# Performance work log

Measured on AMD Instinct MI355X. Metric: run time of the kernel, lower is better.

Reference implementation:

```python
import jax, jax.numpy as jnp
import numpy as np

TOP_K = 2  # active_experts


def setup_inputs() -> dict:
    key = jax.random.key(0)
    k0, k1, k2, k3 = jax.random.split(key, 4)
    B, S, D, E, H = 4, 1024, 2048, 16, 1024
    x = jax.random.normal(k0, (B, S, D), jnp.float32) * 0.02
    Wg = jax.random.normal(k1, (E, D), jnp.float32) * 0.02          # gate: Linear(dim, E, bias=False)
    balance_bias = jnp.zeros((E,), jnp.float32)                      # registered buffer, init zeros
    W1 = jax.random.normal(k2, (E, D, H), jnp.float32) * 0.02        # expert up-proj (no bias)
    W2 = jax.random.normal(k3, (E, H, D), jnp.float32) * 0.02        # expert down-proj (no bias)
    return {"x": x, "Wg": Wg, "balance_bias": balance_bias, "W1": W1, "W2": W2}


def reference(x, Wg, balance_bias, W1, W2):
    B, S, D = x.shape
    E = Wg.shape[0]
    xf = x.reshape(-1, D)                                   # [T, D], T = B*S
    T = xf.shape[0]

    # sigmoid gating with load-balance bias
    gate_logits = xf @ Wg.T                                 # [T, E]
    gate_scores = jax.nn.sigmoid(gate_logits + balance_bias)

    # top-k selection + normalization (matches torch.topk + sum-normalize)
    topk_scores, topk_idx = jax.lax.top_k(gate_scores, TOP_K)
    topk_scores = topk_scores / (topk_scores.sum(-1, keepdims=True) + 1e-6)

    # dense combine weights [T, E]: zero for unselected experts -> identical math
    # to the per-expert masked index_add in the original module
    combine = jnp.zeros((T, E), xf.dtype).at[jnp.arange(T)[:, None], topk_idx].add(topk_scores)

    # per-expert FFN: SiLU(x W1_e) W2_e, weighted-combined across experts
    h = jax.nn.silu(jnp.einsum('td,edh->teh', xf, W1))      # [T, E, H]
    out = jnp.einsum('teh,te,ehd->td', h, combine, W2)      # [T, D]
    return out.reshape(B, S, D)
```

## Files before the change

### kernel.cpp

```cpp
#include <hip/hip_runtime.h>
#include <math.h>

#define T_TOK 4096
#define DDIM  2048
#define HDIM  1024
#define NEXP  16
#define CAP   4096
#define GBM   128
#define GBN   128
#define GBK   64
#define MAX_TILES 80

typedef __attribute__((ext_vector_type(8))) short  short8;
typedef __attribute__((ext_vector_type(4))) float  floatx4;

__device__ __forceinline__ unsigned short f2bf(float f) {
    unsigned int u = __float_as_uint(f);
    u += 0x7fffu + ((u >> 16) & 1u);
    return (unsigned short)(u >> 16);
}
__device__ __forceinline__ float bf2f(unsigned short u) {
    return __uint_as_float((unsigned int)u << 16);
}

__device__ __forceinline__ void gl_lds16(const void* g, void* l) {
    __builtin_amdgcn_global_load_lds(
        (const __attribute__((address_space(1))) unsigned int*)g,
        (__attribute__((address_space(3))) unsigned int*)l,
        16, 0, 0);
}

__global__ __launch_bounds__(256) void prep_kernel(
    const float* __restrict__ x, const float* __restrict__ Wg,
    const float* __restrict__ bias,
    const float* __restrict__ W1, const float* __restrict__ W2,
    unsigned short* __restrict__ W1T, unsigned short* __restrict__ W2T,
    int* __restrict__ counts, int* __restrict__ tok_list,
    int4* __restrict__ tinfo, float2* __restrict__ wcomb,
    unsigned short* __restrict__ xbf)
{
    __shared__ __align__(16) unsigned short Tt[64][72];
    int z = blockIdx.z;

    if (z < 32) {
        const float* src; unsigned short* dst; int K, N, kt, nt;
        if (z < NEXP) {
            K = DDIM; N = HDIM;
            src = W1 + (size_t)z * K * N;
            dst = W1T + (size_t)z * (size_t)N * K;
            kt = blockIdx.y * 64; nt = blockIdx.x * 64;
        } else {
            K = HDIM; N = DDIM;
            src = W2 + (size_t)(z - NEXP) * K * N;
            dst = W2T + (size_t)(z - NEXP) * (size_t)N * K;
            kt = blockIdx.x * 64; nt = blockIdx.y * 64;
        }
        int tid = threadIdx.x;
        int r = tid >> 4, c4 = (tid & 15) * 4;
        const float* s = src + (size_t)kt * N + nt;
#pragma unroll
        for (int i = 0; i < 4; ++i) {
            int rr = r + i * 16;
            float4 v = *(const float4*)(s + (size_t)rr * N + c4);
            Tt[c4 + 0][rr] = f2bf(v.x); Tt[c4 + 1][rr] = f2bf(v.y);
            Tt[c4 + 2][rr] = f2bf(v.z); Tt[c4 + 3][rr] = f2bf(v.w);
        }
        __syncthreads();
        unsigned short* d = dst + (size_t)nt * K + kt;
#pragma unroll
        for (int it = 0; it < 2; ++it) {
            int c = tid + it * 256;
            int n = c >> 3, kc = c & 7;
            short8 v = *(const short8*)&Tt[n][kc * 8];
            *(short8*)(d + (size_t)n * K + kc * 8) = v;
        }
        return;
    }

    int tb   = (z - 32) * 512 + blockIdx.y * 16 + blockIdx.x;
    int wv   = threadIdx.x >> 6;
    int lane = threadIdx.x & 63;
    int t    = tb * 4 + wv;

    const float4* xp4 = (const float4*)x + (size_t)t * (DDIM / 4);
    ushort4* xbp4 = (ushort4*)(xbf + (size_t)t * DDIM);
    const float4* wg4 = (const float4*)Wg;

    float acc[NEXP];
#pragma unroll
    for (int e = 0; e < NEXP; ++e) acc[e] = 0.f;

    for (int it = 0; it < DDIM / 4 / 64; ++it) {
        int d4 = it * 64 + lane;
        float4 xv = xp4[d4];
        ushort4 xs;
        xs.x = f2bf(xv.x); xs.y = f2bf(xv.y);
        xs.z = f2bf(xv.z); xs.w = f2bf(xv.w);
        xbp4[d4] = xs;
#pragma unroll
        for (int e = 0; e < NEXP; ++e) {
            float4 wvv = wg4[e * (DDIM / 4) + d4];
            acc[e] += xv.x * wvv.x + xv.y * wvv.y + xv.z * wvv.z + xv.w * wvv.w;
        }
    }
#pragma unroll
    for (int e = 0; e < NEXP; ++e) {
        float v = acc[e];
#pragma unroll
        for (int off = 32; off > 0; off >>= 1) v += __shfl_xor(v, off, 64);
        acc[e] = v;
    }
    if (lane == 0) {
        float s[NEXP];
#pragma unroll
        for (int e = 0; e < NEXP; ++e)
            s[e] = 1.f / (1.f + expf(-(acc[e] + bias[e])));
        int i0 = 0;
#pragma unroll
        for (int e = 1; e < NEXP; ++e) if (s[e] > s[i0]) i0 = e;
        int i1 = (i0 == 0) ? 1 : 0;
        for (int e = 0; e < NEXP; ++e)
            if (e != i0 && s[e] > s[i1]) i1 = e;
        float denom = s[i0] + s[i1] + 1e-6f;
        int p0 = atomicAdd(&counts[i0], 1);
        tok_list[i0 * CAP + p0] = t;
        int p1 = atomicAdd(&counts[i1], 1);
        tok_list[i1 * CAP + p1] = t;
        tinfo[t] = make_int4(i0, p0, i1, p1);
        wcomb[t] = make_float2(s[i0] / denom, s[i1] / denom);
    }
}

__global__ void scan_kernel(const int* __restrict__ counts, int* __restrict__ offsets,
                            int* __restrict__ ntiles, int* __restrict__ tile_e,
                            int* __restrict__ tile_mt)
{
    if (threadIdx.x == 0 && blockIdx.x == 0) {
        int s = 0, nt = 0;
        for (int e = 0; e < NEXP; ++e) {
            offsets[e] = s;
            int c = counts[e];
            s += c;
            for (int mt = 0; mt * GBM < c; ++mt) {
                tile_e[nt] = e; tile_mt[nt] = mt; ++nt;
            }
        }
        offsets[NEXP] = s;
        *ntiles = nt;
    }
}

__global__ __launch_bounds__(256) void up_gemm(
    const unsigned short* __restrict__ xbf, const unsigned short* __restrict__ W1T,
    const int* __restrict__ counts, const int* __restrict__ offsets,
    const int* __restrict__ ntiles, const int* __restrict__ tile_e,
    const int* __restrict__ tile_mt,
    const int* __restrict__ tok_list, unsigned short* __restrict__ hbuf)
{
    int idx = blockIdx.x;
    if (idx >= *ntiles) return;
    int e   = tile_e[idx];
    int mt  = tile_mt[idx];
    int cnt = counts[e];
    int nbase = blockIdx.y * GBN;

    __shared__ __align__(16) unsigned short As[2][GBM * GBK];
    __shared__ __align__(16) unsigned short Bs[2][GBN * GBK];

    int tid = threadIdx.x, lane = tid & 63, wv = tid >> 6;
    int kcL = ((lane & 7) ^ ((lane >> 3) & 7)) * 8;
    int hbase = offsets[e];

    const unsigned short* gA[4];
    const unsigned short* gB[4];
#pragma unroll
    for (int j = 0; j < 4; ++j) {
        int row = wv * 32 + j * 8 + (lane >> 3);
        int m = mt * GBM + row; if (m >= cnt) m = cnt - 1;
        int tok = tok_list[e * CAP + m];
        gA[j] = xbf + (size_t)tok * DDIM + kcL;
        gB[j] = W1T + ((size_t)e * HDIM + nbase + row) * DDIM + kcL;
    }
    int fr = lane & 15, fq = lane >> 4;
    int wm = (wv & 1) * 64, wn = (wv >> 1) * 64;

    floatx4 acc[4][4];
#pragma unroll
    for (int i = 0; i < 4; ++i)
#pragma unroll
        for (int j = 0; j < 4; ++j) acc[i][j] = (floatx4){0.f, 0.f, 0.f, 0.f};

#pragma unroll
    for (int j = 0; j < 4; ++j)
        gl_lds16(gA[j], &As[0][((wv * 4 + j) * 64 + lane) * 8]);
#pragma unroll
    for (int j = 0; j < 4; ++j)
        gl_lds16(gB[j], &Bs[0][((wv * 4 + j) * 64 + lane) * 8]);

    const int NK = DDIM / GBK;
    for (int i = 0; i < NK; ++i) {
        int cur = i & 1, nxt = cur ^ 1;
        __syncthreads();
        if (i + 1 < NK) {
            int k0 = (i + 1) * GBK;
#pragma unroll
            for (int j = 0; j < 4; ++j)
                gl_lds16(gA[j] + k0, &As[nxt][((wv * 4 + j) * 64 + lane) * 8]);
#pragma unroll
            for (int j = 0; j < 4; ++j)
                gl_lds16(gB[j] + k0, &Bs[nxt][((wv * 4 + j) * 64 + lane) * 8]);
        }
#pragma unroll
        for (int ks = 0; ks < 2; ++ks) {
            short8 af[4], bfr[4];
#pragma unroll
            for (int mi = 0; mi < 4; ++mi) {
                int row = wm + mi * 16 + fr;
                int kcs = (ks * 4 + fq) ^ (row & 7);
                af[mi] = *(const short8*)&As[cur][row * GBK + kcs * 8];
            }
#pragma unroll
            for (int ni = 0; ni < 4; ++ni) {
                int row = wn + ni * 16 + fr;
                int kcs = (ks * 4 + fq) ^ (row & 7);
                bfr[ni] = *(const short8*)&Bs[cur][row * GBK + kcs * 8];
            }
#pragma unroll
            for (int mi = 0; mi < 4; ++mi)
#pragma unroll
                for (int ni = 0; ni < 4; ++ni)
                    acc[mi][ni] = __builtin_amdgcn_mfma_f32_16x16x32_bf16(
                        af[mi], bfr[ni], acc[mi][ni], 0, 0, 0);
        }
    }

#pragma unroll
    for (int mi = 0; mi < 4; ++mi) {
#pragma unroll
        for (int r = 0; r < 4; ++r) {
            int row = wm + mi * 16 + fq * 4 + r;
            int m = mt * GBM + row;
            if (m < cnt) {
                size_t ro = (size_t)(hbase + m) * HDIM + nbase + wn;
#pragma unroll
                for (int ni = 0; ni < 4; ++ni) {
                    float u  = acc[mi][ni][r];
                    float hh = u / (1.f + __expf(-u));
                    hbuf[ro + ni * 16 + fr] = f2bf(hh);
                }
            }
        }
    }
}

__global__ __launch_bounds__(256) void down_gemm(
    const unsigned short* __restrict__ hbuf, const unsigned short* __restrict__ W2T,
    const int* __restrict__ counts, const int* __restrict__ offsets,
    const int* __restrict__ ntiles, const int* __restrict__ tile_e,
    const int* __restrict__ tile_mt,
    unsigned short* __restrict__ ybuf)
{
    int idx = blockIdx.x;
    if (idx >= *ntiles) return;
    int e   = tile_e[idx];
    int mt  = tile_mt[idx];
    int cnt = counts[e];
    int nbase = blockIdx.y * GBN;

    __shared__ __align__(16) unsigned short As[2][GBM * GBK];
    __shared__ __align__(16) unsigned short Bs[2][GBN * GBK];

    int tid = threadIdx.x, lane = tid & 63, wv = tid >> 6;
    int kcL = ((lane & 7) ^ ((lane >> 3) & 7)) * 8;
    int hbase = offsets[e];

    const unsigned short* gA[4];
    const unsigned short* gB[4];
#pragma unroll
    for (int j = 0; j < 4; ++j) {
        int row = wv * 32 + j * 8 + (lane >> 3);
        int m = mt * GBM + row; if (m >= cnt) m = cnt - 1;
        gA[j] = hbuf + (size_t)(hbase + m) * HDIM + kcL;
        gB[j] = W2T + ((size_t)e * DDIM + nbase + row) * HDIM + kcL;
    }
    int fr = lane & 15, fq = lane >> 4;
    int wm = (wv & 1) * 64, wn = (wv >> 1) * 64;

    floatx4 acc[4][4];
#pragma unroll
    for (int i = 0; i < 4; ++i)
#pragma unroll
        for (int j = 0; j < 4; ++j) acc[i][j] = (floatx4){0.f, 0.f, 0.f, 0.f};

#pragma unroll
    for (int j = 0; j < 4; ++j)
        gl_lds16(gA[j], &As[0][((wv * 4 + j) * 64 + lane) * 8]);
#pragma unroll
    for (int j = 0; j < 4; ++j)
        gl_lds16(gB[j], &Bs[0][((wv * 4 + j) * 64 + lane) * 8]);

    const int NK = HDIM / GBK;
    for (int i = 0; i < NK; ++i) {
        int cur = i & 1, nxt = cur ^ 1;
        __syncthreads();
        if (i + 1 < NK) {
            int k0 = (i + 1) * GBK;
#pragma unroll
            for (int j = 0; j < 4; ++j)
                gl_lds16(gA[j] + k0, &As[nxt][((wv * 4 + j) * 64 + lane) * 8]);
#pragma unroll
            for (int j = 0; j < 4; ++j)
                gl_lds16(gB[j] + k0, &Bs[nxt][((wv * 4 + j) * 64 + lane) * 8]);
        }
#pragma unroll
        for (int ks = 0; ks < 2; ++ks) {
            short8 af[4], bfr[4];
#pragma unroll
            for (int mi = 0; mi < 4; ++mi) {
                int row = wm + mi * 16 + fr;
                int kcs = (ks * 4 + fq) ^ (row & 7);
                af[mi] = *(const short8*)&As[cur][row * GBK + kcs * 8];
            }
#pragma unroll
            for (int ni = 0; ni < 4; ++ni) {
                int row = wn + ni * 16 + fr;
                int kcs = (ks * 4 + fq) ^ (row & 7);
                bfr[ni] = *(const short8*)&Bs[cur][row * GBK + kcs * 8];
            }
#pragma unroll
            for (int mi = 0; mi < 4; ++mi)
#pragma unroll
                for (int ni = 0; ni < 4; ++ni)
                    acc[mi][ni] = __builtin_amdgcn_mfma_f32_16x16x32_bf16(
                        af[mi], bfr[ni], acc[mi][ni], 0, 0, 0);
        }
    }

#pragma unroll
    for (int mi = 0; mi < 4; ++mi) {
#pragma unroll
        for (int r = 0; r < 4; ++r) {
            int row = wm + mi * 16 + fq * 4 + r;
            int m = mt * GBM + row;
            if (m < cnt) {
                size_t ro = (size_t)(hbase + m) * DDIM + nbase + wn;
#pragma unroll
                for (int ni = 0; ni < 4; ++ni)
                    ybuf[ro + ni * 16 + fr] = f2bf(acc[mi][ni][r]);
            }
        }
    }
}

__global__ __launch_bounds__(256) void combine_kernel(
    const unsigned short* __restrict__ ybuf, const int* __restrict__ offsets,
    const int4* __restrict__ tinfo, const float2* __restrict__ wcomb,
    float* __restrict__ out)
{
    int t = blockIdx.x;
    int4   ti = tinfo[t];
    float2 w  = wcomb[t];
    int s0 = offsets[ti.x] + ti.y;
    int s1 = offsets[ti.z] + ti.w;
    const ushort4* y0 = (const ushort4*)(ybuf + (size_t)s0 * DDIM);
    const ushort4* y1 = (const ushort4*)(ybuf + (size_t)s1 * DDIM);
    float4* op = (float4*)(out + (size_t)t * DDIM);
#pragma unroll
    for (int i = 0; i < 2; ++i) {
        int c = threadIdx.x + i * 256;
        ushort4 a = y0[c], b = y1[c];
        float4 r;
        r.x = w.x * bf2f(a.x) + w.y * bf2f(b.x);
        r.y = w.x * bf2f(a.y) + w.y * bf2f(b.y);
        r.z = w.x * bf2f(a.z) + w.y * bf2f(b.z);
        r.w = w.x * bf2f(a.w) + w.y * bf2f(b.w);
        op[c] = r;
    }
}

extern "C" void kernel_launch(void* const* d_in, const int* in_sizes, int n_in,
                              void* d_out, int out_size, void* d_ws, size_t ws_size,
                              hipStream_t stream)
{
    const float* x    = (const float*)d_in[0];
    const float* Wg   = (const float*)d_in[1];
    const float* bias = (const float*)d_in[2];
    const float* W1   = (const float*)d_in[3];
    const float* W2   = (const float*)d_in[4];
    float* out = (float*)d_out;

    char* ws = (char*)d_ws;
    int*            counts   = (int*)(ws + 0);
    int*            offsets  = (int*)(ws + 256);
    int*            ntiles   = (int*)(ws + 512);
    int*            tile_e   = (int*)(ws + 512 + 4);
    int*            tile_mt  = (int*)(ws + 512 + 4 + MAX_TILES * 4);
    int*            tok_list = (int*)(ws + 2048);
    int4*           tinfo    = (int4*)(ws + 264192);
    float2*         wcomb    = (float2*)(ws + 329728);
    unsigned short* xbf      = (unsigned short*)(ws + 524288);
    unsigned short* hbuf     = (unsigned short*)(ws + 17301504);
    unsigned short* ybuf     = (unsigned short*)(ws + 34078720);
    unsigned short* W1T      = (unsigned short*)(ws + 67633152);
    unsigned short* W2T      = (unsigned short*)(ws + 134742016);

    hipMemsetAsync(counts, 0, 64, stream);

    prep_kernel<<<dim3(16, 32, 34), 256, 0, stream>>>(
        x, Wg, bias, W1, W2, W1T, W2T, counts, tok_list, tinfo, wcomb, xbf);
    scan_kernel<<<1, 64, 0, stream>>>(counts, offsets, ntiles, tile_e, tile_mt);
    up_gemm<<<dim3(MAX_TILES, HDIM / GBN), 256, 0, stream>>>(
        xbf, W1T, counts, offsets, ntiles, tile_e, tile_mt, tok_list, hbuf);
    down_gemm<<<dim3(MAX_TILES, DDIM / GBN), 256, 0, stream>>>(
        hbuf, W2T, counts, offsets, ntiles, tile_e, tile_mt, ybuf);
    combine_kernel<<<T_TOK, 256, 0, stream>>>(ybuf, offsets, tinfo, wcomb, out);
}
```

Before: 652.2 us.

## Enlarge weight-transpose tiles with swizzled LDS and parallelize routing scan

The weight transpose/bf16 conversion in prep_kernel now processes 256x64 tiles per block instead of 64x64. It packs four k-values per uint2 into an XOR-swizzled LDS layout and writes wider contiguous runs of 512 bytes per row. The gating part now handles 16 tokens per block instead of 4, and the grid shrinks from 17408 blocks to 4352. The single-thread scan kernel is replaced with a wavefront shuffle prefix sum. The aim is to cut the many small blocks, the LDS bank conflicts and the narrow global writes in the weight conversion, at the cost of more LDS per block and possible occupancy or load-balance changes.

```diff
diff --git a/kernel.cpp b/kernel.cpp
--- a/kernel.cpp
+++ b/kernel.cpp
@@ -39,95 +39,114 @@
     int4* __restrict__ tinfo, float2* __restrict__ wcomb,
     unsigned short* __restrict__ xbf)
 {
-    __shared__ __align__(16) unsigned short Tt[64][72];
-    int z = blockIdx.z;
-
-    if (z < 32) {
+    __shared__ __align__(16) unsigned short Ls[64 * 256];
+    int z   = blockIdx.z;
+    int bid = blockIdx.x;
+    int tid = threadIdx.x;
+
+    if (bid < 128) {
         const float* src; unsigned short* dst; int K, N, kt, nt;
         if (z < NEXP) {
             K = DDIM; N = HDIM;
             src = W1 + (size_t)z * K * N;
             dst = W1T + (size_t)z * (size_t)N * K;
-            kt = blockIdx.y * 64; nt = blockIdx.x * 64;
+            kt = bid >> 4; nt = bid & 15;
         } else {
             K = HDIM; N = DDIM;
             src = W2 + (size_t)(z - NEXP) * K * N;
             dst = W2T + (size_t)(z - NEXP) * (size_t)N * K;
-            kt = blockIdx.x * 64; nt = blockIdx.y * 64;
-        }
-        int tid = threadIdx.x;
-        int r = tid >> 4, c4 = (tid & 15) * 4;
-        const float* s = src + (size_t)kt * N + nt;
-#pragma unroll
-        for (int i = 0; i < 4; ++i) {
-            int rr = r + i * 16;
-            float4 v = *(const float4*)(s + (size_t)rr * N + c4);
-            Tt[c4 + 0][rr] = f2bf(v.x); Tt[c4 + 1][rr] = f2bf(v.y);
-            Tt[c4 + 2][rr] = f2bf(v.z); Tt[c4 + 3][rr] = f2bf(v.w);
+            kt = bid >> 5; nt = bid & 31;
+        }
+        int kb = kt * 256, nb = nt * 64;
+        int r = tid >> 4;
+        int c16 = tid & 15;
+        const float* s0 = src + (size_t)kb * N + nb + c16 * 4;
+
+#pragma unroll
+        for (int i4 = 0; i4 < 4; ++i4) {
+            float4 v[4];
+#pragma unroll
+            for (int i = 0; i < 4; ++i)
+                v[i] = *(const float4*)(s0 + (size_t)(i4 * 64 + r * 4 + i) * N);
+#pragma unroll
+            for (int j = 0; j < 4; ++j) {
+                unsigned int lo = (unsigned int)f2bf(((const float*)&v[0])[j])
+                                | ((unsigned int)f2bf(((const float*)&v[1])[j]) << 16);
+                unsigned int hi = (unsigned int)f2bf(((const float*)&v[2])[j])
+                                | ((unsigned int)f2bf(((const float*)&v[3])[j]) << 16);
+                int n  = c16 * 4 + j;
+                int g  = i4 * 16 + r;
+                int gp = g ^ (n & 14);
+                *(uint2*)&Ls[n * 256 + gp * 4] = make_uint2(lo, hi);
+            }
         }
         __syncthreads();
-        unsigned short* d = dst + (size_t)nt * K + kt;
-#pragma unroll
-        for (int it = 0; it < 2; ++it) {
-            int c = tid + it * 256;
-            int n = c >> 3, kc = c & 7;
-            short8 v = *(const short8*)&Tt[n][kc * 8];
-            *(short8*)(d + (size_t)n * K + kc * 8) = v;
+        unsigned short* d0 = dst + (size_t)nb * K + kb;
+#pragma unroll
+        for (int j = 0; j < 8; ++j) {
+            int c = tid + j * 256;
+            int n = c >> 5, a = c & 31;
+            int sp = (2 * a) ^ (n & 14);
+            short8 sv = *(const short8*)&Ls[n * 256 + sp * 4];
+            *(short8*)(d0 + (size_t)n * K + a * 8) = sv;
         }
         return;
     }
 
-    int tb   = (z - 32) * 512 + blockIdx.y * 16 + blockIdx.x;
-    int wv   = threadIdx.x >> 6;
-    int lane = threadIdx.x & 63;
-    int t    = tb * 4 + wv;
-
-    const float4* xp4 = (const float4*)x + (size_t)t * (DDIM / 4);
-    ushort4* xbp4 = (ushort4*)(xbf + (size_t)t * DDIM);
+    int gb   = z * 8 + (bid - 128);
+    int wv   = tid >> 6;
+    int lane = tid & 63;
     const float4* wg4 = (const float4*)Wg;
 
-    float acc[NEXP];
-#pragma unroll
-    for (int e = 0; e < NEXP; ++e) acc[e] = 0.f;
-
-    for (int it = 0; it < DDIM / 4 / 64; ++it) {
-        int d4 = it * 64 + lane;
-        float4 xv = xp4[d4];
-        ushort4 xs;
-        xs.x = f2bf(xv.x); xs.y = f2bf(xv.y);
-        xs.z = f2bf(xv.z); xs.w = f2bf(xv.w);
-        xbp4[d4] = xs;
+    for (int tk = 0; tk < 4; ++tk) {
+        int t = gb * 16 + wv * 4 + tk;
+
+        const float4* xp4 = (const float4*)x + (size_t)t * (DDIM / 4);
+        ushort4* xbp4 = (ushort4*)(xbf + (size_t)t * DDIM);
+
+        float acc[NEXP];
+#pragma unroll
+        for (int e = 0; e < NEXP; ++e) acc[e] = 0.f;
+
+        for (int it = 0; it < DDIM / 4 / 64; ++it) {
+            int d4 = it * 64 + lane;
+            float4 xv = xp4[d4];
+            ushort4 xs;
+            xs.x = f2bf(xv.x); xs.y = f2bf(xv.y);
+            xs.z = f2bf(xv.z); xs.w = f2bf(xv.w);
+            xbp4[d4] = xs;
+#pragma unroll
+            for (int e = 0; e < NEXP; ++e) {
+                float4 wvv = wg4[e * (DDIM / 4) + d4];
+                acc[e] += xv.x * wvv.x + xv.y * wvv.y + xv.z * wvv.z + xv.w * wvv.w;
+            }
+        }
 #pragma unroll
         for (int e = 0; e < NEXP; ++e) {
-            float4 wvv = wg4[e * (DDIM / 4) + d4];
-            acc[e] += xv.x * wvv.x + xv.y * wvv.y + xv.z * wvv.z + xv.w * wvv.w;
-        }
-    }
-#pragma unroll
-    for (int e = 0; e < NEXP; ++e) {
-        float v = acc[e];
-#pragma unroll
-        for (int off = 32; off > 0; off >>= 1) v += __shfl_xor(v, off, 64);
-        acc[e] = v;
-    }
-    if (lane == 0) {
-        float s[NEXP];
-#pragma unroll
-        for (int e = 0; e < NEXP; ++e)
-            s[e] = 1.f / (1.f + expf(-(acc[e] + bias[e])));
-        int i0 = 0;
-#pragma unroll
-        for (int e = 1; e < NEXP; ++e) if (s[e] > s[i0]) i0 = e;
-        int i1 = (i0 == 0) ? 1 : 0;
-        for (int e = 0; e < NEXP; ++e)
-            if (e != i0 && s[e] > s[i1]) i1 = e;
-        float denom = s[i0] + s[i1] + 1e-6f;
-        int p0 = atomicAdd(&counts[i0], 1);
-        tok_list[i0 * CAP + p0] = t;
-        int p1 = atomicAdd(&counts[i1], 1);
-        tok_list[i1 * CAP + p1] = t;
-        tinfo[t] = make_int4(i0, p0, i1, p1);
-        wcomb[t] = make_float2(s[i0] / denom, s[i1] / denom);
+            float v = acc[e];
+#pragma unroll
+            for (int off = 32; off > 0; off >>= 1) v += __shfl_xor(v, off, 64);
+            acc[e] = v;
+        }
+        if (lane == 0) {
+            float s[NEXP];
+#pragma unroll
+            for (int e = 0; e < NEXP; ++e)
+                s[e] = 1.f / (1.f + expf(-(acc[e] + bias[e])));
+            int i0 = 0;
+#pragma unroll
+            for (int e = 1; e < NEXP; ++e) if (s[e] > s[i0]) i0 = e;
+            int i1 = (i0 == 0) ? 1 : 0;
+            for (int e = 0; e < NEXP; ++e)
+                if (e != i0 && s[e] > s[i1]) i1 = e;
+            float denom = s[i0] + s[i1] + 1e-6f;
+            int p0 = atomicAdd(&counts[i0], 1);
+            tok_list[i0 * CAP + p0] = t;
+            int p1 = atomicAdd(&counts[i1], 1);
+            tok_list[i1 * CAP + p1] = t;
+            tinfo[t] = make_int4(i0, p0, i1, p1);
+            wcomb[t] = make_float2(s[i0] / denom, s[i1] / denom);
+        }
     }
 }
 
@@ -135,18 +154,31 @@
                             int* __restrict__ ntiles, int* __restrict__ tile_e,
                             int* __restrict__ tile_mt)
 {
-    if (threadIdx.x == 0 && blockIdx.x == 0) {
-        int s = 0, nt = 0;
-        for (int e = 0; e < NEXP; ++e) {
-            offsets[e] = s;
-            int c = counts[e];
-            s += c;
-            for (int mt = 0; mt * GBM < c; ++mt) {
-                tile_e[nt] = e; tile_mt[nt] = mt; ++nt;
-            }
-        }
-        offsets[NEXP] = s;
-        *ntiles = nt;
+    int lane = threadIdx.x;
+    int c = (lane < NEXP) ? counts[lane] : 0;
+    int incl = c;
+#pragma unroll
+    for (int d = 1; d < 64; d <<= 1) {
+        int v = __shfl_up(incl, d, 64);
+        if (lane >= d) incl += v;
+    }
+    if (lane < NEXP) offsets[lane] = incl - c;
+    if (lane == NEXP - 1) offsets[NEXP] = incl;
+
+    int nt_e = (lane < NEXP) ? ((c + GBM - 1) / GBM) : 0;
+    int tincl = nt_e;
+#pragma unroll
+    for (int d = 1; d < 64; d <<= 1) {
+        int v = __shfl_up(tincl, d, 64);
+        if (lane >= d) tincl += v;
+    }
+    int tbase = tincl - nt_e;
+    if (lane < NEXP) {
+        for (int i = 0; i < nt_e; ++i) {
+            tile_e[tbase + i]  = lane;
+            tile_mt[tbase + i] = i;
+        }
+        if (lane == NEXP - 1) *ntiles = tbase + nt_e;
     }
 }
 
@@ -406,7 +438,7 @@
 
     hipMemsetAsync(counts, 0, 64, stream);
 
-    prep_kernel<<<dim3(16, 32, 34), 256, 0, stream>>>(
+    prep_kernel<<<dim3(136, 1, 32), 256, 0, stream>>>(
         x, Wg, bias, W1, W2, W1T, W2T, counts, tok_list, tinfo, wcomb, xbf);
     scan_kernel<<<1, 64, 0, stream>>>(counts, offsets, ntiles, tile_e, tile_mt);
     up_gemm<<<dim3(MAX_TILES, HDIM / GBN), 256, 0, stream>>>(
```

New measurement: 647.7 us. About the same (-0.7%).
